# Kernel optimization log

Measured on AMD Instinct MI355X. Metric: run time of the kernel, lower is better.

## Reference

```python
import jax, jax.numpy as jnp
import numpy as np

E, H, T_MAX = 1024, 16, 2048
HS = E // H
EPS = 1e-5


def _layernorm(x, g, b):
    m = jnp.mean(x, axis=-1, keepdims=True)
    v = jnp.mean(jnp.square(x - m), axis=-1, keepdims=True)
    return (x - m) * jax.lax.rsqrt(v + EPS) * g + b


def setup_inputs() -> dict:
    key = jax.random.key(0)
    ks = jax.random.split(key, 8)
    B, T = 2, 2048
    s = 0.02
    return {
        "x": jax.random.normal(ks[0], (B, T, E), jnp.float32),
        "ln1_g": jnp.ones((E,), jnp.float32),
        "ln1_b": jnp.zeros((E,), jnp.float32),
        "Wk": jax.random.normal(ks[1], (H, E, HS), jnp.float32) * s,  # stacked per-head key weights (x @ Wk)
        "Wv": jax.random.normal(ks[2], (H, E, HS), jnp.float32) * s,
        "Wproj": jax.random.normal(ks[3], (E, E), jnp.float32) * s,
        "bproj": jnp.zeros((E,), jnp.float32),
        "ln2_g": jnp.ones((E,), jnp.float32),
        "ln2_b": jnp.zeros((E,), jnp.float32),
        "W1": jax.random.normal(ks[4], (E, 4 * E), jnp.float32) * s,
        "b1": jnp.zeros((4 * E,), jnp.float32),
        "W2": jax.random.normal(ks[5], (4 * E, E), jnp.float32) * s,
        "b2": jnp.zeros((E,), jnp.float32),
    }


def reference(x, ln1_g, ln1_b, Wk, Wv, Wproj, bproj, ln2_g, ln2_b, W1, b1, W2, b2):
    B, T, C = x.shape
    h = _layernorm(x, ln1_g, ln1_b)
    # NOTE: original code uses the KEY projection for both q and k (q = self.key(x))
    k = jnp.einsum('bte,hed->bhtd', h, Wk)
    q = k
    wei = jnp.einsum('bhtd,bhsd->bhts', q, k) * (C ** -0.5)  # scale by full n_embd, as in source
    causal = jnp.tril(jnp.ones((T, T), bool))
    wei = jnp.where(causal, wei, -jnp.inf)
    # source applies softmax over dim=1 (the query/row axis of the TxT matrix)
    wei = jax.nn.softmax(wei, axis=2)
    v = jnp.einsum('bte,hed->bhtd', h, Wv)
    attn = jnp.einsum('bhts,bhsd->bhtd', wei, v)          # [B,H,T,HS]
    attn = attn.transpose(0, 2, 1, 3).reshape(B, T, C)    # concat heads
    x = x + attn @ Wproj + bproj
    h2 = _layernorm(x, ln2_g, ln2_b)
    x = x + jax.nn.relu(h2 @ W1 + b1) @ W2 + b2
    return x
```

## Files before the change

kernel.cpp:

```cpp
#include <hip/hip_runtime.h>

using bf16x8 = __attribute__((ext_vector_type(8))) __bf16;
using f32x4  = __attribute__((ext_vector_type(4))) float;

__device__ __forceinline__ f32x4 mfma16(bf16x8 a, bf16x8 b, f32x4 c) {
  return __builtin_amdgcn_mfma_f32_16x16x32_bf16(a, b, c, 0, 0, 0);
}

__device__ __forceinline__ unsigned short f2bf(float f) {
  union { float f; unsigned int u; } x; x.f = f;
  unsigned int u = x.u + 0x7FFFu + ((x.u >> 16) & 1u);
  return (unsigned short)(u >> 16);
}

__device__ __forceinline__ unsigned int cvtpk_bf16(float lo, float hi) {
  unsigned int r;
  asm("v_cvt_pk_bf16_f32 %0, %1, %2" : "=v"(r) : "v"(lo), "v"(hi));
  return r;
}

__device__ __forceinline__ float fexp2(float x) {
#if __has_builtin(__builtin_amdgcn_exp2f)
  return __builtin_amdgcn_exp2f(x);
#else
  float r; asm("v_exp_f32 %0, %1" : "=v"(r) : "v"(x)); return r;
#endif
}

__device__ __forceinline__ void gl_lds16(const unsigned short* g, unsigned short* l) {
  __builtin_amdgcn_global_load_lds(
      (__attribute__((address_space(1))) void*)(g),
      (__attribute__((address_space(3))) void*)(l), 16, 0, 0);
}

__device__ __forceinline__ bf16x8 rdsw64(const unsigned short* base, int r, int ch) {
  int c = ch ^ (r & 7);
  return *reinterpret_cast<const bf16x8*>(base + ((size_t)r * 8 + c) * 8);
}

__global__ __launch_bounds__(256) void transpose_cvt(const float* __restrict__ in,
                                                     unsigned short* __restrict__ out,
                                                     int R, int C) {
  __shared__ float t[32][33];
  int b = blockIdx.z;
  const float* inb = in + (size_t)b * R * C;
  unsigned short* outb = out + (size_t)b * R * C;
  int tx = threadIdx.x & 31, ty = threadIdx.x >> 5;
  int c0 = blockIdx.x * 32, r0 = blockIdx.y * 32;
#pragma unroll
  for (int i = 0; i < 4; ++i)
    t[ty + i * 8][tx] = inb[(size_t)(r0 + ty + i * 8) * C + c0 + tx];
  __syncthreads();
#pragma unroll
  for (int i = 0; i < 4; ++i)
    outb[(size_t)(c0 + ty + i * 8) * R + r0 + tx] = f2bf(t[tx][ty + i * 8]);
}

__global__ __launch_bounds__(256) void ln_bf16(const float* __restrict__ x,
                                               const float* __restrict__ g,
                                               const float* __restrict__ bta,
                                               unsigned short* __restrict__ out) {
  int row = blockIdx.x, tid = threadIdx.x;
  float4 v = reinterpret_cast<const float4*>(x + (size_t)row * 1024)[tid];
  float s = v.x + v.y + v.z + v.w;
  float s2 = v.x * v.x + v.y * v.y + v.z * v.z + v.w * v.w;
#pragma unroll
  for (int m = 1; m < 64; m <<= 1) { s += __shfl_xor(s, m); s2 += __shfl_xor(s2, m); }
  __shared__ float red[8];
  int w = tid >> 6;
  if ((tid & 63) == 0) { red[w] = s; red[w + 4] = s2; }
  __syncthreads();
  s  = red[0] + red[1] + red[2] + red[3];
  s2 = red[4] + red[5] + red[6] + red[7];
  float mean = s * (1.f / 1024.f);
  float var  = s2 * (1.f / 1024.f) - mean * mean;
  float rstd = rsqrtf(var + 1e-5f);
  float4 gv = reinterpret_cast<const float4*>(g)[tid];
  float4 bv = reinterpret_cast<const float4*>(bta)[tid];
  ushort4 o;
  o.x = f2bf((v.x - mean) * rstd * gv.x + bv.x);
  o.y = f2bf((v.y - mean) * rstd * gv.y + bv.y);
  o.z = f2bf((v.z - mean) * rstd * gv.z + bv.z);
  o.w = f2bf((v.w - mean) * rstd * gv.w + bv.w);
  reinterpret_cast<ushort4*>(out + (size_t)row * 1024)[tid] = o;
}

#define KSCL 0.04508422f

template<int TM, int MODE>
__global__ __launch_bounds__(256) void gemm_bf16(const unsigned short* __restrict__ A,
                                                 const unsigned short* __restrict__ Bt,
                                                 void* __restrict__ Cout,
                                                 unsigned short* __restrict__ Cout2,
                                                 const float* __restrict__ bias,
                                                 const float* __restrict__ resid,
                                                 const float* __restrict__ scvec,
                                                 int M, int N, int K) {
  constexpr int MI  = TM / 32;
  constexpr int ALD = TM / 32;
  constexpr int NLD = ALD + 4;
  __shared__ __align__(16) unsigned short Sh[2][(TM + 128) * 64];
  int tid = threadIdx.x;
  int lane = tid & 63, w = tid >> 6;
  int l15 = lane & 15, lh = lane >> 4;
  int wr = (w >> 1) * (TM / 2), wc = (w & 1) * 64;
  int nblk = N >> 7;
  int rows = M / TM;
  int bm, bn;
  if ((rows & 7) == 0) {
    int bid = blockIdx.x;
    int xcd = bid & 7, g = bid >> 3;
    bm = xcd * (rows >> 3) + g / nblk;
    bn = g % nblk;
  } else {
    bm = blockIdx.x / nblk; bn = blockIdx.x % nblk;
  }
  const unsigned short* Asrc[ALD];
  const unsigned short* Bsrc[4];
#pragma unroll
  for (int j = 0; j < ALD; ++j) {
    int row = j * 32 + (tid >> 3);
    int ch  = (tid & 7) ^ (row & 7);
    Asrc[j] = A + (size_t)(bm * TM + row) * K + ch * 8;
  }
#pragma unroll
  for (int j = 0; j < 4; ++j) {
    int row = j * 32 + (tid >> 3);
    int ch  = (tid & 7) ^ (row & 7);
    Bsrc[j] = Bt + (size_t)(bn * 128 + row) * K + ch * 8;
  }
  f32x4 acc[MI][4] = {};
  int NT = K >> 6;
  {
#pragma unroll
    for (int j = 0; j < ALD; ++j) gl_lds16(Asrc[j], &Sh[0][(j * 256 + tid) * 8]);
#pragma unroll
    for (int j = 0; j < 4; ++j)  gl_lds16(Bsrc[j], &Sh[0][TM * 64 + (j * 256 + tid) * 8]);
  }
  for (int t = 0; t < NT; ++t) {
    int cur = t & 1;
    const unsigned short* Asc = &Sh[cur][0];
    const unsigned short* Bsc = &Sh[cur][TM * 64];
    if (t + 1 < NT) {
      int k0 = (t + 1) << 6;
      unsigned short* Asn = &Sh[cur ^ 1][0];
      unsigned short* Bsn = &Sh[cur ^ 1][TM * 64];
#pragma unroll
      for (int j = 0; j < ALD; ++j) gl_lds16(Asrc[j] + k0, Asn + (j * 256 + tid) * 8);
#pragma unroll
      for (int j = 0; j < 4; ++j)  gl_lds16(Bsrc[j] + k0, Bsn + (j * 256 + tid) * 8);
      asm volatile("s_waitcnt vmcnt(%0)" :: "i"(NLD) : "memory");
    } else {
      asm volatile("s_waitcnt vmcnt(0)" ::: "memory");
    }
    __builtin_amdgcn_s_barrier();
    bf16x8 af[MI][2], bfr[4][2];
#pragma unroll
    for (int i = 0; i < MI; ++i)
#pragma unroll
      for (int kk = 0; kk < 2; ++kk)
        af[i][kk] = rdsw64(Asc, wr + i * 16 + l15, kk * 4 + lh);
#pragma unroll
    for (int i = 0; i < 4; ++i)
#pragma unroll
      for (int kk = 0; kk < 2; ++kk)
        bfr[i][kk] = rdsw64(Bsc, wc + i * 16 + l15, kk * 4 + lh);
    __builtin_amdgcn_s_setprio(1);
#pragma unroll
    for (int kk = 0; kk < 2; ++kk)
#pragma unroll
      for (int mi = 0; mi < MI; ++mi)
#pragma unroll
        for (int ni = 0; ni < 4; ++ni)
          acc[mi][ni] = mfma16(af[mi][kk], bfr[ni][kk], acc[mi][ni]);
    __builtin_amdgcn_s_setprio(0);
    __builtin_amdgcn_s_barrier();
  }
  unsigned short* Sh0 = &Sh[0][0];
  if constexpr (MODE == 3) {
#pragma unroll
    for (int mi = 0; mi < MI; ++mi) {
#pragma unroll
      for (int ni = 0; ni < 4; ++ni) {
        int tl = wr + mi * 16 + lh * 4;
        int dl = wc + ni * 16 + l15;
        int colg = bn * 128 + dl;
        int bb = bm >> 5, hh = colg >> 6;
        const float* sp = scvec + (size_t)(bb * 16 + hh) * 2048 + (bm & 31) * 64 + tl;
        float4 rs = *reinterpret_cast<const float4*>(sp);
        unsigned int p0 = f2bf(acc[mi][ni][0] * rs.x) | ((unsigned int)f2bf(acc[mi][ni][1] * rs.y) << 16);
        unsigned int p1 = f2bf(acc[mi][ni][2] * rs.z) | ((unsigned int)f2bf(acc[mi][ni][3] * rs.w) << 16);
        uint2 pk = {p0, p1};
        *reinterpret_cast<uint2*>(&Sh0[dl * 64 + (tl ^ ((dl & 7) << 3))]) = pk;
      }
    }
    __syncthreads();
    int dr = tid >> 1, th = (tid & 1) * 32;
    int bb = bm >> 5, tbase = (bm & 31) * 64;
    size_t colg = bn * 128 + dr;
    unsigned short* Vt = (unsigned short*)Cout;
#pragma unroll
    for (int j = 0; j < 4; ++j) {
      int t = th + j * 8;
      int4 v = *reinterpret_cast<const int4*>(&Sh0[dr * 64 + (t ^ ((dr & 7) << 3))]);
      *reinterpret_cast<int4*>(&Vt[((size_t)bb * 1024 + colg) * 2048 + tbase + t]) = v;
    }
  } else {
#pragma unroll
    for (int mi = 0; mi < MI; ++mi) {
#pragma unroll
      for (int ni = 0; ni < 4; ++ni) {
        int row0 = bm * TM + wr + mi * 16 + lh * 4;
        int col  = bn * 128 + wc + ni * 16 + l15;
        float bv = (MODE == 2) ? 0.f : bias[col];
#pragma unroll
        for (int r = 0; r < 4; ++r) {
          int row = row0 + r;
          float v = acc[mi][ni][r] + bv;
          if constexpr (MODE == 0) {
            v += resid[(size_t)row * N + col];
            ((float*)Cout)[(size_t)row * N + col] = v;
          } else if constexpr (MODE == 1) {
            v = fmaxf(v, 0.f);
            ((unsigned short*)Cout)[(size_t)row * N + col] = f2bf(v);
          } else {
            ((unsigned short*)Cout)[(size_t)row * N + col] = f2bf(v);
            Cout2[(size_t)row * N + col] = f2bf(v * KSCL);
          }
        }
      }
    }
  }
}

__global__ __launch_bounds__(512) void attn_stats(const unsigned short* __restrict__ Kb,
                                                  const unsigned short* __restrict__ Kbs,
                                                  float* __restrict__ colrcp) {
  __shared__ __align__(16) unsigned short Kt[2][64 * 64];
  int bid = blockIdx.x;
  int q = bid >> 8, x = (bid >> 5) & 7, bh = bid & 31;
  int b = bh >> 4, h = bh & 15;
  int sb = q ? (15 - x) : x;
  int tid = threadIdx.x, lane = tid & 63, w = tid >> 6;
  int l15 = lane & 15, lh = lane >> 4;
  int s0 = sb * 128, sw = s0 + w * 16;
  const unsigned short* Kp  = Kb  + ((size_t)b * 2048) * 1024 + h * 64;
  const unsigned short* Kps = Kbs + ((size_t)b * 2048) * 1024 + h * 64;
  bf16x8 as[2];
#pragma unroll
  for (int kc = 0; kc < 2; ++kc)
    as[kc] = *reinterpret_cast<const bf16x8*>(Kp + (size_t)(sw + l15) * 1024 + kc * 32 + (lh << 3));
  int srow = tid >> 3;
  int sch  = (tid & 7) ^ (srow & 7);
  const unsigned short* ksrc = Kps + (size_t)srow * 1024 + sch * 8;
  gl_lds16(ksrc + (size_t)s0 * 1024, &Kt[0][tid * 8]);
  __syncthreads();
  float l[4] = {0.f, 0.f, 0.f, 0.f};
  int nt = 32 - 2 * sb;
  for (int it = 0; it < nt; ++it) {
    int t0 = s0 + it * 64;
    int cur = it & 1;
    if (it + 1 < nt)
      gl_lds16(ksrc + (size_t)(t0 + 64) * 1024, &Kt[cur ^ 1][tid * 8]);
    if (t0 + 63 >= sw) {
      bool dmask = (t0 < sw + 16);
#pragma unroll
      for (int tf = 0; tf < 4; ++tf) {
        int tr = tf * 16 + l15;
        bf16x8 bt0 = rdsw64(&Kt[cur][0], tr, lh);
        bf16x8 bt1 = rdsw64(&Kt[cur][0], tr, 4 + lh);
        f32x4 z = {};
        f32x4 sa = mfma16(as[1], bt1, mfma16(as[0], bt0, z));
        int tg = t0 + tr;
#pragma unroll
        for (int r = 0; r < 4; ++r) {
          float e = fexp2(sa[r]);
          if (dmask) { int sg = sw + lh * 4 + r; e = (tg >= sg) ? e : 0.f; }
          l[r] += e;
        }
      }
    }
    __syncthreads();
  }
#pragma unroll
  for (int m = 1; m < 16; m <<= 1)
#pragma unroll
    for (int r = 0; r < 4; ++r)
      l[r] += __shfl_xor(l[r], m);
  if (l15 == 0) {
#pragma unroll
    for (int r = 0; r < 4; ++r)
      colrcp[(size_t)bh * 2048 + sw + lh * 4 + r] = 1.f / l[r];
  }
}

__global__ __launch_bounds__(512) void attn_pv(const unsigned short* __restrict__ Kb,
                                               const unsigned short* __restrict__ Kbs,
                                               const unsigned short* __restrict__ Vt,
                                               unsigned short* __restrict__ attn) {
  __shared__ __align__(16) unsigned short Ks[2][64 * 64];
  __shared__ __align__(16) unsigned short Vs[3][64 * 64];
  __shared__ __align__(16) unsigned short Pl[8][2][16][68];
  int bid = blockIdx.x;
  int q = bid >> 8, x = (bid >> 5) & 7, bh = bid & 31;
  int b = bh >> 4, h = bh & 15;
  int tb = q ? x : (15 - x);
  int tid = threadIdx.x, lane = tid & 63, w = tid >> 6;
  int l15 = lane & 15, lh = lane >> 4;
  int t0 = tb * 128, tw = t0 + w * 16;
  const unsigned short* Kp  = Kb  + ((size_t)b * 2048) * 1024 + h * 64;
  const unsigned short* Kps = Kbs + ((size_t)b * 2048) * 1024 + h * 64;
  const unsigned short* Vp  = Vt + (size_t)bh * 64 * 2048;
  bf16x8 at[2];
#pragma unroll
  for (int kc = 0; kc < 2; ++kc)
    at[kc] = *reinterpret_cast<const bf16x8*>(Kp + (size_t)(tw + l15) * 1024 + kc * 32 + (lh << 3));
  int srow = tid >> 3;
  int sch  = (tid & 7) ^ (srow & 7);
  const unsigned short* ksrc = Kps + (size_t)srow * 1024 + sch * 8;
  const unsigned short* vsrc = Vp + (size_t)srow * 2048 + sch * 8;
  int nt = 2 * tb + 2;
  gl_lds16(ksrc, &Ks[0][tid * 8]);
  gl_lds16(vsrc, &Vs[0][tid * 8]);
  __syncthreads();
  f32x4 acc[4] = {};
  for (int it = 0; it < nt; ++it) {
    int s0 = it * 64;
    const unsigned short* ksCur = &Ks[it & 1][0];
    if (it + 1 < nt) {
      gl_lds16(ksrc + (size_t)(s0 + 64) * 1024, &Ks[(it + 1) & 1][tid * 8]);
      gl_lds16(vsrc + (s0 + 64), &Vs[(it + 1) % 3][tid * 8]);
    }
    if (s0 <= tw + 15) {
      bool dmask = (s0 + 63 > tw);
#pragma unroll
      for (int sf = 0; sf < 4; ++sf) {
        int sr = sf * 16 + l15;
        bf16x8 ks0 = rdsw64(ksCur, sr, lh);
        bf16x8 ks1 = rdsw64(ksCur, sr, 4 + lh);
        f32x4 z = {};
        f32x4 sa = mfma16(ks1, at[1], mfma16(ks0, at[0], z));
        float pe[4];
#pragma unroll
        for (int r = 0; r < 4; ++r) {
          float p = fexp2(sa[r]);
          if (dmask) {
            int sg = s0 + sf * 16 + lh * 4 + r;
            int tg = tw + l15;
            p = (sg <= tg) ? p : 0.f;
          }
          pe[r] = p;
        }
        unsigned int u0 = cvtpk_bf16(pe[0], pe[1]);
        unsigned int u1 = cvtpk_bf16(pe[2], pe[3]);
        unsigned long long pk = (unsigned long long)u0 | ((unsigned long long)u1 << 32);
        *reinterpret_cast<unsigned long long*>(&Pl[w][it & 1][l15][sf * 16 + lh * 4]) = pk;
      }
    }
    if (it > 0) {
      int pit = it - 1;
      if (pit * 64 <= tw + 15) {
        const unsigned short* vsPrev = &Vs[pit % 3][0];
#pragma unroll
        for (int c2 = 0; c2 < 2; ++c2) {
          bf16x8 pa = *reinterpret_cast<const bf16x8*>(&Pl[w][pit & 1][l15][c2 * 32 + (lh << 3)]);
#pragma unroll
          for (int nf = 0; nf < 4; ++nf) {
            int dr = nf * 16 + l15;
            bf16x8 vb = rdsw64(vsPrev, dr, c2 * 4 + lh);
            acc[nf] = mfma16(pa, vb, acc[nf]);
          }
        }
      }
    }
    __syncthreads();
  }
  {
    int pit = nt - 1;
    if (pit * 64 <= tw + 15) {
      const unsigned short* vsPrev = &Vs[pit % 3][0];
#pragma unroll
      for (int c2 = 0; c2 < 2; ++c2) {
        bf16x8 pa = *reinterpret_cast<const bf16x8*>(&Pl[w][pit & 1][l15][c2 * 32 + (lh << 3)]);
#pragma unroll
        for (int nf = 0; nf < 4; ++nf) {
          int dr = nf * 16 + l15;
          bf16x8 vb = rdsw64(vsPrev, dr, c2 * 4 + lh);
          acc[nf] = mfma16(pa, vb, acc[nf]);
        }
      }
    }
  }
#pragma unroll
  for (int nf = 0; nf < 4; ++nf)
#pragma unroll
    for (int r = 0; r < 4; ++r) {
      int t = tw + lh * 4 + r;
      attn[(size_t)(b * 2048 + t) * 1024 + h * 64 + nf * 16 + l15] = f2bf(acc[nf][r]);
    }
}

extern "C" void kernel_launch(void* const* d_in, const int* in_sizes, int n_in,
                              void* d_out, int out_size, void* d_ws, size_t ws_size,
                              hipStream_t stream) {
  (void)in_sizes; (void)n_in; (void)out_size; (void)ws_size;
  const float* x     = (const float*)d_in[0];
  const float* ln1_g = (const float*)d_in[1];
  const float* ln1_b = (const float*)d_in[2];
  const float* Wk    = (const float*)d_in[3];
  const float* Wv    = (const float*)d_in[4];
  const float* Wproj = (const float*)d_in[5];
  const float* bproj = (const float*)d_in[6];
  const float* ln2_g = (const float*)d_in[7];
  const float* ln2_b = (const float*)d_in[8];
  const float* W1    = (const float*)d_in[9];
  const float* b1    = (const float*)d_in[10];
  const float* W2    = (const float*)d_in[11];
  const float* b2    = (const float*)d_in[12];
  float* out = (float*)d_out;

  char* ws = (char*)d_ws;
  size_t off = 0;
  auto alloc = [&](size_t bytes) { void* p = ws + off; off += (bytes + 255) & ~(size_t)255; return p; };
  unsigned short* bufA = (unsigned short*)alloc((size_t)4096 * 1024 * 2);
  unsigned short* wk_t = (unsigned short*)alloc((size_t)1024 * 1024 * 2);
  unsigned short* wv_t = (unsigned short*)alloc((size_t)1024 * 1024 * 2);
  unsigned short* wp_t = (unsigned short*)alloc((size_t)1024 * 1024 * 2);
  unsigned short* w1_t = (unsigned short*)alloc((size_t)1024 * 4096 * 2);
  unsigned short* w2_t = (unsigned short*)alloc((size_t)4096 * 1024 * 2);
  unsigned short* Kb   = (unsigned short*)alloc((size_t)4096 * 1024 * 2);
  unsigned short* Kbs  = (unsigned short*)alloc((size_t)4096 * 1024 * 2);
  unsigned short* Vt   = (unsigned short*)alloc((size_t)4096 * 1024 * 2);
  float* colrcp = (float*)alloc((size_t)32 * 2048 * 4);
  float* y      = (float*)alloc((size_t)4096 * 1024 * 4);
  unsigned short* act = (unsigned short*)alloc((size_t)4096 * 4096 * 2);

  dim3 b256(256), b512(512);
  transpose_cvt<<<dim3(2, 32, 16), b256, 0, stream>>>(Wk, wk_t, 1024, 64);
  transpose_cvt<<<dim3(2, 32, 16), b256, 0, stream>>>(Wv, wv_t, 1024, 64);
  transpose_cvt<<<dim3(32, 32, 1), b256, 0, stream>>>(Wproj, wp_t, 1024, 1024);
  transpose_cvt<<<dim3(128, 32, 1), b256, 0, stream>>>(W1, w1_t, 1024, 4096);
  transpose_cvt<<<dim3(32, 128, 1), b256, 0, stream>>>(W2, w2_t, 4096, 1024);

  ln_bf16<<<4096, b256, 0, stream>>>(x, ln1_g, ln1_b, bufA);
  gemm_bf16<64, 2><<<512, b256, 0, stream>>>(bufA, wk_t, Kb, Kbs, nullptr, nullptr, nullptr, 4096, 1024, 1024);
  attn_stats<<<512, b512, 0, stream>>>(Kb, Kbs, colrcp);
  gemm_bf16<64, 3><<<512, b256, 0, stream>>>(bufA, wv_t, Vt, nullptr, nullptr, nullptr, colrcp, 4096, 1024, 1024);
  attn_pv<<<512, b512, 0, stream>>>(Kb, Kbs, Vt, bufA);
  gemm_bf16<64, 0><<<512, b256, 0, stream>>>(bufA, wp_t, y, nullptr, bproj, x, nullptr, 4096, 1024, 1024);
  ln_bf16<<<4096, b256, 0, stream>>>(y, ln2_g, ln2_b, bufA);
  gemm_bf16<128, 1><<<1024, b256, 0, stream>>>(bufA, w1_t, act, nullptr, b1, nullptr, nullptr, 4096, 4096, 1024);
  gemm_bf16<64, 0><<<512, b256, 0, stream>>>(act, w2_t, out, nullptr, b2, y, nullptr, 4096, 1024, 4096);
}
```

Before: 231.0 us.

## Fuse K and V projections into one GEMM, move softmax scaling into attention

K and V projections now run as a single GEMM with N=2048 over a concatenated transposed weight. Blocks in the first half write K row-major and blocks in the second half write transposed V. The separate pre-scaled K copy is dropped: the score scale is applied in fp32 inside the attention kernels, and the column reciprocal normalization moves from the V epilogue into attn_pv. This removes one kernel launch, the extra K-scaled buffer write, and the dependency of the V GEMM on attn_stats. In exchange, attn_pv does an extra float4 load and multiply per score tile.

After: 237.4 us. +2.7%, slower.

```diff
diff --git a/kernel.cpp b/kernel.cpp
--- a/kernel.cpp
+++ b/kernel.cpp
@@ -91,10 +91,8 @@
 __global__ __launch_bounds__(256) void gemm_bf16(const unsigned short* __restrict__ A,
                                                  const unsigned short* __restrict__ Bt,
                                                  void* __restrict__ Cout,
-                                                 unsigned short* __restrict__ Cout2,
                                                  const float* __restrict__ bias,
                                                  const float* __restrict__ resid,
-                                                 const float* __restrict__ scvec,
                                                  int M, int N, int K) {
   constexpr int MI  = TM / 32;
   constexpr int ALD = TM / 32;
@@ -177,33 +175,43 @@
     __builtin_amdgcn_s_barrier();
   }
   unsigned short* Sh0 = &Sh[0][0];
-  if constexpr (MODE == 3) {
-#pragma unroll
-    for (int mi = 0; mi < MI; ++mi) {
-#pragma unroll
-      for (int ni = 0; ni < 4; ++ni) {
-        int tl = wr + mi * 16 + lh * 4;
-        int dl = wc + ni * 16 + l15;
-        int colg = bn * 128 + dl;
-        int bb = bm >> 5, hh = colg >> 6;
-        const float* sp = scvec + (size_t)(bb * 16 + hh) * 2048 + (bm & 31) * 64 + tl;
-        float4 rs = *reinterpret_cast<const float4*>(sp);
-        unsigned int p0 = f2bf(acc[mi][ni][0] * rs.x) | ((unsigned int)f2bf(acc[mi][ni][1] * rs.y) << 16);
-        unsigned int p1 = f2bf(acc[mi][ni][2] * rs.z) | ((unsigned int)f2bf(acc[mi][ni][3] * rs.w) << 16);
-        uint2 pk = {p0, p1};
-        *reinterpret_cast<uint2*>(&Sh0[dl * 64 + (tl ^ ((dl & 7) << 3))]) = pk;
-      }
-    }
-    __syncthreads();
-    int dr = tid >> 1, th = (tid & 1) * 32;
-    int bb = bm >> 5, tbase = (bm & 31) * 64;
-    size_t colg = bn * 128 + dr;
-    unsigned short* Vt = (unsigned short*)Cout;
-#pragma unroll
-    for (int j = 0; j < 4; ++j) {
-      int t = th + j * 8;
-      int4 v = *reinterpret_cast<const int4*>(&Sh0[dr * 64 + (t ^ ((dr & 7) << 3))]);
-      *reinterpret_cast<int4*>(&Vt[((size_t)bb * 1024 + colg) * 2048 + tbase + t]) = v;
+  if constexpr (MODE == 4) {
+    if (bn < 8) {
+#pragma unroll
+      for (int mi = 0; mi < MI; ++mi)
+#pragma unroll
+        for (int ni = 0; ni < 4; ++ni) {
+          int row0 = bm * TM + wr + mi * 16 + lh * 4;
+          int col  = bn * 128 + wc + ni * 16 + l15;
+#pragma unroll
+          for (int r = 0; r < 4; ++r)
+            ((unsigned short*)Cout)[(size_t)(row0 + r) * 1024 + col] = f2bf(acc[mi][ni][r]);
+        }
+    } else {
+#pragma unroll
+      for (int mi = 0; mi < MI; ++mi) {
+#pragma unroll
+        for (int ni = 0; ni < 4; ++ni) {
+          int tl = wr + mi * 16 + lh * 4;
+          int dl = wc + ni * 16 + l15;
+          unsigned int p0 = f2bf(acc[mi][ni][0]) | ((unsigned int)f2bf(acc[mi][ni][1]) << 16);
+          unsigned int p1 = f2bf(acc[mi][ni][2]) | ((unsigned int)f2bf(acc[mi][ni][3]) << 16);
+          uint2 pk = {p0, p1};
+          *reinterpret_cast<uint2*>(&Sh0[dl * 64 + (tl ^ ((dl & 7) << 3))]) = pk;
+        }
+      }
+      __syncthreads();
+      int dr = tid >> 1, th = (tid & 1) * 32;
+      int bb = bm >> 5, tbase = (bm & 31) * 64;
+      size_t colg = (bn - 8) * 128 + dr;
+      unsigned short* Vt = (unsigned short*)Cout;
+      Vt += (size_t)4096 * 1024;
+#pragma unroll
+      for (int j = 0; j < 4; ++j) {
+        int t = th + j * 8;
+        int4 v = *reinterpret_cast<const int4*>(&Sh0[dr * 64 + (t ^ ((dr & 7) << 3))]);
+        *reinterpret_cast<int4*>(&Vt[((size_t)bb * 1024 + colg) * 2048 + tbase + t]) = v;
+      }
     }
   } else {
 #pragma unroll
@@ -212,7 +220,7 @@
       for (int ni = 0; ni < 4; ++ni) {
         int row0 = bm * TM + wr + mi * 16 + lh * 4;
         int col  = bn * 128 + wc + ni * 16 + l15;
-        float bv = (MODE == 2) ? 0.f : bias[col];
+        float bv = bias[col];
 #pragma unroll
         for (int r = 0; r < 4; ++r) {
           int row = row0 + r;
@@ -220,12 +228,9 @@
           if constexpr (MODE == 0) {
             v += resid[(size_t)row * N + col];
             ((float*)Cout)[(size_t)row * N + col] = v;
-          } else if constexpr (MODE == 1) {
+          } else {
             v = fmaxf(v, 0.f);
             ((unsigned short*)Cout)[(size_t)row * N + col] = f2bf(v);
-          } else {
-            ((unsigned short*)Cout)[(size_t)row * N + col] = f2bf(v);
-            Cout2[(size_t)row * N + col] = f2bf(v * KSCL);
           }
         }
       }
@@ -234,7 +239,6 @@
 }
 
 __global__ __launch_bounds__(512) void attn_stats(const unsigned short* __restrict__ Kb,
-                                                  const unsigned short* __restrict__ Kbs,
                                                   float* __restrict__ colrcp) {
   __shared__ __align__(16) unsigned short Kt[2][64 * 64];
   int bid = blockIdx.x;
@@ -244,15 +248,14 @@
   int tid = threadIdx.x, lane = tid & 63, w = tid >> 6;
   int l15 = lane & 15, lh = lane >> 4;
   int s0 = sb * 128, sw = s0 + w * 16;
-  const unsigned short* Kp  = Kb  + ((size_t)b * 2048) * 1024 + h * 64;
-  const unsigned short* Kps = Kbs + ((size_t)b * 2048) * 1024 + h * 64;
+  const unsigned short* Kp = Kb + ((size_t)b * 2048) * 1024 + h * 64;
   bf16x8 as[2];
 #pragma unroll
   for (int kc = 0; kc < 2; ++kc)
     as[kc] = *reinterpret_cast<const bf16x8*>(Kp + (size_t)(sw + l15) * 1024 + kc * 32 + (lh << 3));
   int srow = tid >> 3;
   int sch  = (tid & 7) ^ (srow & 7);
-  const unsigned short* ksrc = Kps + (size_t)srow * 1024 + sch * 8;
+  const unsigned short* ksrc = Kp + (size_t)srow * 1024 + sch * 8;
   gl_lds16(ksrc + (size_t)s0 * 1024, &Kt[0][tid * 8]);
   __syncthreads();
   float l[4] = {0.f, 0.f, 0.f, 0.f};
@@ -274,7 +277,7 @@
         int tg = t0 + tr;
 #pragma unroll
         for (int r = 0; r < 4; ++r) {
-          float e = fexp2(sa[r]);
+          float e = fexp2(sa[r] * KSCL);
           if (dmask) { int sg = sw + lh * 4 + r; e = (tg >= sg) ? e : 0.f; }
           l[r] += e;
         }
@@ -295,7 +298,7 @@
 }
 
 __global__ __launch_bounds__(512) void attn_pv(const unsigned short* __restrict__ Kb,
-                                               const unsigned short* __restrict__ Kbs,
+                                               const float* __restrict__ colrcp,
                                                const unsigned short* __restrict__ Vt,
                                                unsigned short* __restrict__ attn) {
   __shared__ __align__(16) unsigned short Ks[2][64 * 64];
@@ -308,16 +311,16 @@
   int tid = threadIdx.x, lane = tid & 63, w = tid >> 6;
   int l15 = lane & 15, lh = lane >> 4;
   int t0 = tb * 128, tw = t0 + w * 16;
-  const unsigned short* Kp  = Kb  + ((size_t)b * 2048) * 1024 + h * 64;
-  const unsigned short* Kps = Kbs + ((size_t)b * 2048) * 1024 + h * 64;
-  const unsigned short* Vp  = Vt + (size_t)bh * 64 * 2048;
+  const unsigned short* Kp = Kb + ((size_t)b * 2048) * 1024 + h * 64;
+  const unsigned short* Vp = Vt + (size_t)bh * 64 * 2048;
+  const float* cr = colrcp + (size_t)bh * 2048;
   bf16x8 at[2];
 #pragma unroll
   for (int kc = 0; kc < 2; ++kc)
     at[kc] = *reinterpret_cast<const bf16x8*>(Kp + (size_t)(tw + l15) * 1024 + kc * 32 + (lh << 3));
   int srow = tid >> 3;
   int sch  = (tid & 7) ^ (srow & 7);
-  const unsigned short* ksrc = Kps + (size_t)srow * 1024 + sch * 8;
+  const unsigned short* ksrc = Kp + (size_t)srow * 1024 + sch * 8;
   const unsigned short* vsrc = Vp + (size_t)srow * 2048 + sch * 8;
   int nt = 2 * tb + 2;
   gl_lds16(ksrc, &Ks[0][tid * 8]);
@@ -340,10 +343,12 @@
         bf16x8 ks1 = rdsw64(ksCur, sr, 4 + lh);
         f32x4 z = {};
         f32x4 sa = mfma16(ks1, at[1], mfma16(ks0, at[0], z));
+        float4 rs4 = *reinterpret_cast<const float4*>(cr + s0 + sf * 16 + lh * 4);
+        const float* rsp = reinterpret_cast<const float*>(&rs4);
         float pe[4];
 #pragma unroll
         for (int r = 0; r < 4; ++r) {
-          float p = fexp2(sa[r]);
+          float p = fexp2(sa[r] * KSCL) * rsp[r];
           if (dmask) {
             int sg = s0 + sf * 16 + lh * 4 + r;
             int tg = tw + l15;
@@ -422,33 +427,30 @@
   char* ws = (char*)d_ws;
   size_t off = 0;
   auto alloc = [&](size_t bytes) { void* p = ws + off; off += (bytes + 255) & ~(size_t)255; return p; };
-  unsigned short* bufA = (unsigned short*)alloc((size_t)4096 * 1024 * 2);
-  unsigned short* wk_t = (unsigned short*)alloc((size_t)1024 * 1024 * 2);
-  unsigned short* wv_t = (unsigned short*)alloc((size_t)1024 * 1024 * 2);
-  unsigned short* wp_t = (unsigned short*)alloc((size_t)1024 * 1024 * 2);
-  unsigned short* w1_t = (unsigned short*)alloc((size_t)1024 * 4096 * 2);
-  unsigned short* w2_t = (unsigned short*)alloc((size_t)4096 * 1024 * 2);
-  unsigned short* Kb   = (unsigned short*)alloc((size_t)4096 * 1024 * 2);
-  unsigned short* Kbs  = (unsigned short*)alloc((size_t)4096 * 1024 * 2);
-  unsigned short* Vt   = (unsigned short*)alloc((size_t)4096 * 1024 * 2);
+  unsigned short* bufA  = (unsigned short*)alloc((size_t)4096 * 1024 * 2);
+  unsigned short* wkv_t = (unsigned short*)alloc((size_t)2048 * 1024 * 2);
+  unsigned short* wp_t  = (unsigned short*)alloc((size_t)1024 * 1024 * 2);
+  unsigned short* w1_t  = (unsigned short*)alloc((size_t)1024 * 4096 * 2);
+  unsigned short* w2_t  = (unsigned short*)alloc((size_t)4096 * 1024 * 2);
+  unsigned short* Kb    = (unsigned short*)alloc((size_t)4096 * 1024 * 2);
+  unsigned short* Vt    = (unsigned short*)alloc((size_t)4096 * 1024 * 2);
   float* colrcp = (float*)alloc((size_t)32 * 2048 * 4);
   float* y      = (float*)alloc((size_t)4096 * 1024 * 4);
   unsigned short* act = (unsigned short*)alloc((size_t)4096 * 4096 * 2);
 
   dim3 b256(256), b512(512);
-  transpose_cvt<<<dim3(2, 32, 16), b256, 0, stream>>>(Wk, wk_t, 1024, 64);
-  transpose_cvt<<<dim3(2, 32, 16), b256, 0, stream>>>(Wv, wv_t, 1024, 64);
+  transpose_cvt<<<dim3(2, 32, 16), b256, 0, stream>>>(Wk, wkv_t, 1024, 64);
+  transpose_cvt<<<dim3(2, 32, 16), b256, 0, stream>>>(Wv, wkv_t + (size_t)1024 * 1024, 1024, 64);
   transpose_cvt<<<dim3(32, 32, 1), b256, 0, stream>>>(Wproj, wp_t, 1024, 1024);
   transpose_cvt<<<dim3(128, 32, 1), b256, 0, stream>>>(W1, w1_t, 1024, 4096);
   transpose_cvt<<<dim3(32, 128, 1), b256, 0, stream>>>(W2, w2_t, 4096, 1024);
 
   ln_bf16<<<4096, b256, 0, stream>>>(x, ln1_g, ln1_b, bufA);
-  gemm_bf16<64, 2><<<512, b256, 0, stream>>>(bufA, wk_t, Kb, Kbs, nullptr, nullptr, nullptr, 4096, 1024, 1024);
-  attn_stats<<<512, b512, 0, stream>>>(Kb, Kbs, colrcp);
-  gemm_bf16<64, 3><<<512, b256, 0, stream>>>(bufA, wv_t, Vt, nullptr, nullptr, nullptr, colrcp, 4096, 1024, 1024);
-  attn_pv<<<512, b512, 0, stream>>>(Kb, Kbs, Vt, bufA);
-  gemm_bf16<64, 0><<<512, b256, 0, stream>>>(bufA, wp_t, y, nullptr, bproj, x, nullptr, 4096, 1024, 1024);
+  gemm_bf16<64, 4><<<1024, b256, 0, stream>>>(bufA, wkv_t, Kb, nullptr, nullptr, 4096, 2048, 1024);
+  attn_stats<<<512, b512, 0, stream>>>(Kb, colrcp);
+  attn_pv<<<512, b512, 0, stream>>>(Kb, colrcp, Vt, bufA);
+  gemm_bf16<64, 0><<<512, b256, 0, stream>>>(bufA, wp_t, y, bproj, x, 4096, 1024, 1024);
   ln_bf16<<<4096, b256, 0, stream>>>(y, ln2_g, ln2_b, bufA);
-  gemm_bf16<128, 1><<<1024, b256, 0, stream>>>(bufA, w1_t, act, nullptr, b1, nullptr, nullptr, 4096, 4096, 1024);
-  gemm_bf16<64, 0><<<512, b256, 0, stream>>>(act, w2_t, out, nullptr, b2, y, nullptr, 4096, 1024, 4096);
-}
+  gemm_bf16<128, 1><<<1024, b256, 0, stream>>>(bufA, w1_t, act, b1, nullptr, 4096, 4096, 1024);
+  gemm_bf16<64, 0><<<512, b256, 0, stream>>>(act, w2_t, out, b2, y, 4096, 1024, 4096);
+}
```
